# Kernel tuning notes

Measured on AMD Instinct MI355X. Metric: run time of the kernel, lower is better.

## Reference

```python
import jax, jax.numpy as jnp
import numpy as np

B, S, D, H, DH, FF = 2, 2048, 1024, 16, 64, 4096
EPS = 1e-6


def setup_inputs() -> dict:
    key = jax.random.key(0)
    ks = jax.random.split(key, 12)
    s = lambda fan: 1.0 / np.sqrt(fan)
    return {
        "x": jax.random.normal(ks[0], (B, S, D), dtype=jnp.float32),
        "mask": jax.random.randint(ks[1], (B, S), 0, 2).astype(bool),
        "Wq": jax.random.normal(ks[2], (D, H * DH), dtype=jnp.float32) * s(D),
        "Wk": jax.random.normal(ks[3], (D, H * DH), dtype=jnp.float32) * s(D),
        "Wv": jax.random.normal(ks[4], (D, H * DH), dtype=jnp.float32) * s(D),
        "Wo": jax.random.normal(ks[5], (H * DH, D), dtype=jnp.float32) * s(H * DH),
        "bo": jnp.zeros((D,), dtype=jnp.float32),
        "W1": jax.random.normal(ks[6], (D, FF), dtype=jnp.float32) * s(D),
        "b1": jnp.zeros((FF,), dtype=jnp.float32),
        "W2": jax.random.normal(ks[7], (FF, D), dtype=jnp.float32) * s(FF),
        "b2": jnp.zeros((D,), dtype=jnp.float32),
        "g1": jnp.ones((D,), dtype=jnp.float32),   # layer_norm1 target_std
        "m1": jnp.zeros((D,), dtype=jnp.float32),  # layer_norm1 target_mean
        "g2": jnp.ones((D,), dtype=jnp.float32),
        "m2": jnp.zeros((D,), dtype=jnp.float32),
    }


def layer_norm(x, g, m):
    mu = jnp.mean(x, axis=-1, keepdims=True)
    xc = x - mu
    std = jnp.sqrt(jnp.mean(xc * xc, axis=-1, keepdims=True) + EPS)
    return g * xc / std + m


def reference(x, mask, Wq, Wk, Wv, Wo, bo, W1, b1, W2, b2, g1, m1, g2, m2):
    # --- multi-head self-attention (no proj bias) ---
    q = (x @ Wq).reshape(B, S, H, DH)
    k = (x @ Wk).reshape(B, S, H, DH)
    v = (x @ Wv).reshape(B, S, H, DH)
    scores = jnp.einsum("bqhd,bkhd->bhqk", q, k) / np.sqrt(DH)  # [B,H,S,S]
    scores = jnp.where(mask[:, None, None, :], -jnp.inf, scores)
    att = jax.nn.softmax(scores, axis=-1)
    ctx = jnp.einsum("bhqk,bkhd->bqhd", att, v).reshape(B, S, H * DH)
    attn_out = ctx @ Wo + bo
    # --- post-LN residual block (pre_ln=False, dropouts=0 in eval) ---
    x1 = layer_norm(attn_out + x, g1, m1)
    ff = jax.nn.relu(x1 @ W1 + b1) @ W2 + b2
    return layer_norm(ff + x1, g2, m2)
```

## Files before the change

### kernel.cpp

```cpp
#include <hip/hip_runtime.h>
#include <hip/hip_bf16.h>


typedef __bf16 bf16;
typedef __bf16 bf16x8 __attribute__((ext_vector_type(8)));
typedef __bf16 bf16x4 __attribute__((ext_vector_type(4)));
typedef float  f32x4  __attribute__((ext_vector_type(4)));
typedef float  f32x16 __attribute__((ext_vector_type(16)));
typedef unsigned u32x2 __attribute__((ext_vector_type(2)));
typedef unsigned u32x4 __attribute__((ext_vector_type(4)));

#define DEVI __device__ __forceinline__

constexpr int S_LEN  = 2048;
constexpr int NTOK   = 4096;
constexpr int DMODEL = 1024;
constexpr int NFF    = 4096;
constexpr float SCALE2 = 0.125f * 1.44269504088896f;
constexpr float MASKV2 = -30000.0f;

DEVI void gld16(const void* g, void* l) {
  __builtin_amdgcn_global_load_lds((const __attribute__((address_space(1))) void*)g,
                                   (__attribute__((address_space(3))) void*)l, 16, 0, 0);
}

DEVI f32x4 mfma16(bf16x8 a, bf16x8 b, f32x4 c) {
  return __builtin_amdgcn_mfma_f32_16x16x32_bf16(a, b, c, 0, 0, 0);
}
DEVI f32x16 mfma32(bf16x8 a, bf16x8 b, f32x16 c) {
  return __builtin_amdgcn_mfma_f32_32x32x16_bf16(a, b, c, 0, 0, 0);
}
DEVI unsigned cvtpk(float lo, float hi) {
  unsigned d;
  asm("v_cvt_pk_bf16_f32 %0, %1, %2" : "=v"(d) : "v"(lo), "v"(hi));
  return d;
}
DEVI void plswap(unsigned &a, unsigned &b) {
#if __has_builtin(__builtin_amdgcn_permlane32_swap)
  u32x2 r = __builtin_amdgcn_permlane32_swap(a, b, false, false);
  a = r[0]; b = r[1];
#else
  asm volatile("v_permlane32_swap_b32 %0, %1" : "+v"(a), "+v"(b));
#endif
}
DEVI float fexp2(float x) {
#if __has_builtin(__builtin_amdgcn_exp2f)
  return __builtin_amdgcn_exp2f(x);
#else
  return exp2f(x);
#endif
}
#define M3(a, b, c) fmaxf(fmaxf(a, b), c)

template <int MODE>
__global__ __launch_bounds__(512) void gemm8p(
    const bf16* __restrict__ A, const bf16* __restrict__ Bt,
    void* __restrict__ out, const float* __restrict__ bias, int N, int nx)
{
  __shared__ bf16 lds8[65536];
  const int tid = threadIdx.x, lane = tid & 63, w = tid >> 6;
  const int wr = w >> 2, wc = w & 3;
  const int li16 = lane & 15, hi4 = lane >> 4, l7 = lane & 7, b3 = (lane >> 3) & 1;

  const int id = blockIdx.x;
  const int t2 = id >> 3;
  const int bx = t2 % nx;
  const int by = (id & 7) * 2 + t2 / nx;
  const int brow = by * 256, bcol = bx * 256;

  const int srow = tid >> 3;
  const int ssl  = (tid & 7) ^ ((srow ^ (srow >> 3)) & 7);
  const bf16* aG = A  + ((size_t)(brow + srow)) * 1024 + ssl * 8;
  const bf16* bG = Bt + ((size_t)(bcol + srow)) * 1024 + ssl * 8;

  auto STA = [&](int buf, int t, int h) {
    const bf16* g = aG + t * 64 + (size_t)(h * 2) * 65536;
    gld16(g,         lds8 + buf * 32768 + (h * 2) * 4096 + w * 512);
    gld16(g + 65536, lds8 + buf * 32768 + (h * 2 + 1) * 4096 + w * 512);
  };
  auto STB = [&](int buf, int t, int h) {
    const bf16* g = bG + t * 64 + (size_t)(h * 2) * 65536;
    gld16(g,         lds8 + buf * 32768 + 16384 + (h * 2) * 4096 + w * 512);
    gld16(g + 65536, lds8 + buf * 32768 + 16384 + (h * 2 + 1) * 4096 + w * 512);
  };

  const int sa[4] = { l7 ^ ((0 + b3) & 7), l7 ^ ((2 + b3) & 7),
                      l7 ^ ((4 + b3) & 7), l7 ^ ((6 + b3) & 7) };
  const int sb[2] = { l7 ^ ((wc * 4 + 0 + b3) & 7), l7 ^ ((wc * 4 + 2 + b3) & 7) };

  f32x4 acc[2][2][4][2] = {};

#define VM4 asm volatile("s_waitcnt vmcnt(4)" ::: "memory")
#define VM0 asm volatile("s_waitcnt vmcnt(0)" ::: "memory")
#define NOP ((void)0)
#define PH(BUF, MQ, NQ, STG, WAIT) do {                                          \
    bf16x8 af[4][2], bg[2][2];                                                   \
    _Pragma("unroll") for (int m = 0; m < 4; ++m) {                              \
      const bf16* rp = lds8 + (BUF) * 32768 +                                    \
                       ((MQ) * 128 + wr * 64 + m * 16 + li16) * 64;              \
      _Pragma("unroll") for (int ks = 0; ks < 2; ++ks)                           \
        af[m][ks] = *(const bf16x8*)(rp + ((ks * 4 + hi4) ^ sa[m]) * 8);         \
    }                                                                            \
    _Pragma("unroll") for (int n = 0; n < 2; ++n) {                              \
      const bf16* rp = lds8 + (BUF) * 32768 + 16384 +                            \
                       ((NQ) * 128 + wc * 32 + n * 16 + li16) * 64;              \
      _Pragma("unroll") for (int ks = 0; ks < 2; ++ks)                           \
        bg[n][ks] = *(const bf16x8*)(rp + ((ks * 4 + hi4) ^ sb[n]) * 8);         \
    }                                                                            \
    STG;                                                                         \
    asm volatile("s_barrier" ::: "memory");                                      \
    __builtin_amdgcn_s_setprio(1);                                               \
    _Pragma("unroll") for (int m = 0; m < 4; ++m)                                \
      _Pragma("unroll") for (int n = 0; n < 2; ++n)                              \
        _Pragma("unroll") for (int ks = 0; ks < 2; ++ks)                         \
          acc[MQ][NQ][m][n] = mfma16(af[m][ks], bg[n][ks], acc[MQ][NQ][m][n]);   \
    __builtin_amdgcn_s_setprio(0);                                               \
    __builtin_amdgcn_sched_barrier(0);                                           \
    WAIT;                                                                        \
    asm volatile("s_barrier" ::: "memory");                                      \
  } while (0)

  STA(0, 0, 0); STA(0, 0, 1); STB(0, 0, 0); STB(0, 0, 1);
  STA(1, 1, 0); STB(1, 1, 0);
  VM4;
  asm volatile("s_barrier" ::: "memory");

  for (int it = 0; it < 7; ++it) {
    const int t = 2 * it;
    PH(0, 0, 0, STA(1, t + 1, 1), NOP);
    PH(0, 0, 1, STB(1, t + 1, 1), NOP);
    PH(0, 1, 0, STA(0, t + 2, 0), NOP);
    PH(0, 1, 1, STB(0, t + 2, 0), VM4);
    PH(1, 0, 0, STA(0, t + 2, 1), NOP);
    PH(1, 0, 1, STB(0, t + 2, 1), NOP);
    PH(1, 1, 0, STA(1, t + 3, 0), NOP);
    PH(1, 1, 1, STB(1, t + 3, 0), VM4);
  }
  PH(0, 0, 0, STA(1, 15, 1), NOP);
  PH(0, 0, 1, STB(1, 15, 1), NOP);
  PH(0, 1, 0, NOP, NOP);
  PH(0, 1, 1, NOP, VM0);
  PH(1, 0, 0, NOP, NOP);
  PH(1, 0, 1, NOP, NOP);
  PH(1, 1, 0, NOP, NOP);
  PH(1, 1, 1, NOP, NOP);
#undef PH
#undef VM4
#undef VM0
#undef NOP

  const size_t plane = (size_t)NTOK * DMODEL;
#pragma unroll
  for (int mq = 0; mq < 2; ++mq)
#pragma unroll
    for (int nq = 0; nq < 2; ++nq)
#pragma unroll
      for (int m = 0; m < 4; ++m)
#pragma unroll
        for (int n = 0; n < 2; ++n)
#pragma unroll
          for (int j = 0; j < 4; ++j) {
            const int row = brow + mq * 128 + wr * 64 + m * 16 + hi4 * 4 + j;
            const int col = bcol + nq * 128 + wc * 32 + n * 16 + li16;
            const float v = acc[mq][nq][m][n][j];
            if (MODE == 3) {
              const float t = v + bias[col];
              ((bf16*)out)[(size_t)row * N + col] = (bf16)fmaxf(t, 0.0f);
            } else {
              const int b = row >> 11, s = row & 2047;
              const int which = col >> 10, c = col & 1023, h = c >> 6, d = c & 63;
              bf16* qkv = (bf16*)out;
              if (which == 0)
                qkv[(((size_t)(b * 16 + h)) * 2048 + s) * 64 + d] = (bf16)(v * SCALE2);
              else if (which == 1)
                (qkv + plane)[(((size_t)(b * 16 + h)) * 2048 + s) * 64 + d] = (bf16)v;
              else
                (qkv + 2 * plane)[(((size_t)(b * 16 + h)) * 64 + d) * 2048 + s] = (bf16)v;
            }
          }
}

template <int MODE>
__global__ __launch_bounds__(256) void gemm_bt(
    const bf16* __restrict__ A, const bf16* __restrict__ Bt,
    void* __restrict__ out, const float* __restrict__ bias,
    int M, int N, int ld, int Kc, int nx, int ny)
{
  __shared__ bf16 As[128 * 32];
  __shared__ bf16 Bs[128 * 32];
  const int tid  = threadIdx.x;
  const int lane = tid & 63, w = tid >> 6;
  const int wr = w >> 1, wc = w & 1;

  const int id  = blockIdx.x;
  const int xcd = id & 7;
  int t2 = id >> 3;
  const int bx = t2 % nx;  t2 /= nx;
  const int ppx = ny >> 3;
  const int kz = t2 / ppx;
  const int by = xcd * ppx + (t2 % ppx);
  const int brow = by * 128, bcol = bx * 128;

  const bf16* Ag = A  + (size_t)(brow + w * 32 + (lane >> 2)) * ld + kz * Kc + (lane & 3) * 8;
  const bf16* Bg = Bt + (size_t)(bcol + w * 32 + (lane >> 2)) * ld + kz * Kc + (lane & 3) * 8;
  bf16* AsW = As + w * 1024;
  bf16* BsW = Bs + w * 1024;

  f32x4 acc[4][4] = {};

  for (int k0 = 0; k0 < Kc; k0 += 32) {
    gld16(Ag + k0,                    AsW);
    gld16(Ag + k0 + (size_t)16 * ld,  AsW + 512);
    gld16(Bg + k0,                    BsW);
    gld16(Bg + k0 + (size_t)16 * ld,  BsW + 512);
    __syncthreads();

    bf16x8 af[4], bfr[4];
#pragma unroll
    for (int m = 0; m < 4; ++m)
      af[m] = *(const bf16x8*)&As[(wr * 64 + m * 16 + (lane & 15)) * 32 + (lane >> 4) * 8];
#pragma unroll
    for (int n = 0; n < 4; ++n)
      bfr[n] = *(const bf16x8*)&Bs[(wc * 64 + n * 16 + (lane & 15)) * 32 + (lane >> 4) * 8];
    __builtin_amdgcn_s_setprio(1);
#pragma unroll
    for (int m = 0; m < 4; ++m)
#pragma unroll
      for (int n = 0; n < 4; ++n)
        acc[m][n] = mfma16(af[m], bfr[n], acc[m][n]);
    __builtin_amdgcn_s_setprio(0);
    __syncthreads();
  }

#pragma unroll
  for (int m = 0; m < 4; ++m)
#pragma unroll
    for (int n = 0; n < 4; ++n)
#pragma unroll
      for (int r = 0; r < 4; ++r) {
        const int row = brow + wr * 64 + m * 16 + (lane >> 4) * 4 + r;
        const int col = bcol + wc * 64 + n * 16 + (lane & 15);
        ((float*)out)[(size_t)kz * M * N + (size_t)row * N + col] = acc[m][n][r];
      }
}

__global__ __launch_bounds__(512) void attn_k(
    const bf16* __restrict__ q, const bf16* __restrict__ k,
    const bf16* __restrict__ vt, const unsigned* __restrict__ mbits,
    bf16* __restrict__ ctx)
{
  __shared__ __align__(16) char smem[36864];
  bf16* Kl = (bf16*)smem;
  bf16* Vl = (bf16*)(smem + 16384);
  const int tid = threadIdx.x, lane = tid & 63, w = tid >> 6;
  const int hi = lane >> 5, li = lane & 31;
  const int id = blockIdx.x;
  const int j = id >> 3;
  const int bh = (id & 7) * 4 + (j & 3);
  const int b = bh >> 4, h = bh & 15;
  const int qbase = (j >> 2) * 256 + w * 32;

  bf16x8 qf[4];
  {
    const bf16* qp = q + ((size_t)bh * S_LEN + qbase + li) * 64 + hi * 8;
#pragma unroll
    for (int c = 0; c < 4; ++c) qf[c] = *(const bf16x8*)(qp + c * 16);
  }
  const u32x4 onesu = {0x3F803F80u, 0x3F803F80u, 0x3F803F80u, 0x3F803F80u};
  const bf16x8 onesv = __builtin_bit_cast(bf16x8, onesu);

  f32x16 o[2] = {};
  f32x16 acc1 = {};
  float mrun = -3.0e38f;

  const int srow = w * 8 + (lane >> 3);
  const int sslot = (lane & 7) ^ ((srow ^ (srow >> 3)) & 7);
  const bf16* kg = k  + ((size_t)bh * S_LEN + srow) * 64 + sslot * 8;
  const bf16* vg = vt + ((size_t)bh * 64 + srow) * S_LEN + sslot * 8;

  gld16(kg, Kl + w * 512);
  gld16(vg, Vl + w * 512);
  __syncthreads();

  int buf = 0;
  for (int kt = 0; kt < 32; ++kt) {
    const int nb = buf ^ 1;
    if (kt + 1 < 32) {
      gld16(kg + (size_t)(kt + 1) * 4096, Kl + nb * 4096 + w * 512);
      gld16(vg + (kt + 1) * 64,           Vl + nb * 4096 + w * 512);
    }
    const unsigned mw0 = mbits[b * 64 + kt * 2]     >> (hi * 4);
    const unsigned mw1 = mbits[b * 64 + kt * 2 + 1] >> (hi * 4);
    const bf16* Kb = Kl + buf * 4096;
    const bf16* Vb = Vl + buf * 4096;

    float sc[2][16];
#pragma unroll
    for (int kblk = 0; kblk < 2; ++kblk) {
      const int key = kblk * 32 + li;
      const unsigned swb = ((key ^ (key >> 3)) & 7) << 4;
      const char* kr = (const char*)Kb + key * 128;
      f32x16 st = {};
      __builtin_amdgcn_s_setprio(1);
#pragma unroll
      for (int c = 0; c < 4; ++c) {
        const bf16x8 kf = *(const bf16x8*)(kr + ((unsigned)(c * 32 + hi * 16) ^ swb));
        st = mfma32(kf, qf[c], st);
      }
      __builtin_amdgcn_s_setprio(0);
      const unsigned msh = kblk ? mw1 : mw0;
#pragma unroll
      for (int r = 0; r < 16; ++r) {
        const int cb = (r & 3) + 8 * (r >> 2);
        sc[kblk][r] = (msh & (1u << cb)) ? MASKV2 : st[r];
      }
    }

    const float* sf = &sc[0][0];
    float m0[11];
#pragma unroll
    for (int i3 = 0; i3 < 10; ++i3) m0[i3] = M3(sf[i3 * 3], sf[i3 * 3 + 1], sf[i3 * 3 + 2]);
    m0[10] = fmaxf(sf[30], sf[31]);
    float tm = fmaxf(fmaxf(M3(m0[0], m0[1], m0[2]), M3(m0[3], m0[4], m0[5])),
                     fmaxf(M3(m0[6], m0[7], m0[8]), fmaxf(m0[9], m0[10])));
    tm = fmaxf(tm, __shfl_xor(tm, 32, 64));

    if (!__all(tm <= mrun + 11.0f)) {
      const float mnew = fmaxf(mrun, tm);
      const float alpha = fexp2(mrun - mnew);
      mrun = mnew;
      o[0] *= alpha;
      o[1] *= alpha;
      acc1[0] = acc1[0] * alpha;
    }
#pragma unroll
    for (int kblk = 0; kblk < 2; ++kblk)
#pragma unroll
      for (int r = 0; r < 16; ++r)
        sc[kblk][r] = fexp2(sc[kblk][r] - mrun);

    bf16x8 pa[4];
#pragma unroll
    for (int kblk = 0; kblk < 2; ++kblk)
#pragma unroll
      for (int hf = 0; hf < 2; ++hf) {
        unsigned A = cvtpk(sc[kblk][hf * 8 + 0], sc[kblk][hf * 8 + 1]);
        unsigned B = cvtpk(sc[kblk][hf * 8 + 2], sc[kblk][hf * 8 + 3]);
        unsigned C = cvtpk(sc[kblk][hf * 8 + 4], sc[kblk][hf * 8 + 5]);
        unsigned D = cvtpk(sc[kblk][hf * 8 + 6], sc[kblk][hf * 8 + 7]);
        plswap(A, C);
        plswap(B, D);
        const u32x4 t = {A, B, C, D};
        pa[kblk * 2 + hf] = __builtin_bit_cast(bf16x8, t);
      }

#pragma unroll
    for (int dblk = 0; dblk < 2; ++dblk) {
      const int d = dblk * 32 + li;
      const unsigned swb = ((d ^ (d >> 3)) & 7) << 4;
      const char* vr = (const char*)Vb + d * 128;
      __builtin_amdgcn_s_setprio(1);
#pragma unroll
      for (int ch = 0; ch < 4; ++ch) {
        const bf16x8 vf = *(const bf16x8*)(vr + ((unsigned)(ch * 32 + hi * 16) ^ swb));
        o[dblk] = mfma32(vf, pa[ch], o[dblk]);
      }
      __builtin_amdgcn_s_setprio(0);
    }
#pragma unroll
    for (int ch = 0; ch < 4; ++ch) acc1 = mfma32(onesv, pa[ch], acc1);
    __syncthreads();
    buf = nb;
  }

  const float rl = 1.0f / acc1[0];
  char* Ep = smem + w * 4608;
#pragma unroll
  for (int dblk = 0; dblk < 2; ++dblk)
#pragma unroll
    for (int g = 0; g < 4; ++g) {
      const unsigned lo = cvtpk(o[dblk][4 * g + 0] * rl, o[dblk][4 * g + 1] * rl);
      const unsigned hw = cvtpk(o[dblk][4 * g + 2] * rl, o[dblk][4 * g + 3] * rl);
      const int d0 = 8 * g + 4 * hi + 32 * dblk;
      *(unsigned long long*)(Ep + li * 144 + d0 * 2) =
          ((unsigned long long)hw << 32) | (unsigned long long)lo;
    }
#pragma unroll
  for (int i = 0; i < 4; ++i) {
    const int r = (lane >> 3) + 8 * i;
    const bf16x8 vv = *(const bf16x8*)(Ep + r * 144 + (lane & 7) * 16);
    *(bf16x8*)(ctx + ((size_t)b * S_LEN + qbase + r) * DMODEL + h * 64 + (lane & 7) * 8) = vv;
  }
}

template <int NPART, int RB>
__global__ __launch_bounds__(256) void ln_k(
    const float* __restrict__ parts, const float* __restrict__ bias,
    const void* __restrict__ resid, const float* __restrict__ gam,
    const float* __restrict__ bet, float* __restrict__ of, bf16* __restrict__ ob)
{
  const int row = blockIdx.x, t = threadIdx.x;
  float4 v = ((const float4*)(parts + (size_t)row * DMODEL))[t];
#pragma unroll
  for (int p = 1; p < NPART; ++p) {
    const float4 u = ((const float4*)(parts + ((size_t)p * NTOK + row) * DMODEL))[t];
    v.x += u.x; v.y += u.y; v.z += u.z; v.w += u.w;
  }
  {
    const float4 b4 = ((const float4*)bias)[t];
    float4 r4;
    if (RB) {
      const bf16x4 rb = *(const bf16x4*)((const bf16*)resid + (size_t)row * DMODEL + t * 4);
      r4.x = (float)rb[0]; r4.y = (float)rb[1]; r4.z = (float)rb[2]; r4.w = (float)rb[3];
    } else {
      r4 = ((const float4*)((const float*)resid + (size_t)row * DMODEL))[t];
    }
    v.x += b4.x + r4.x; v.y += b4.y + r4.y; v.z += b4.z + r4.z; v.w += b4.w + r4.w;
  }
  float s  = v.x + v.y + v.z + v.w;
  float s2 = v.x * v.x + v.y * v.y + v.z * v.z + v.w * v.w;
#pragma unroll
  for (int off = 1; off < 64; off <<= 1) {
    s  += __shfl_xor(s, off, 64);
    s2 += __shfl_xor(s2, off, 64);
  }
  __shared__ float ps[4], ps2[4];
  if ((t & 63) == 0) { ps[t >> 6] = s; ps2[t >> 6] = s2; }
  __syncthreads();
  s  = ps[0] + ps[1] + ps[2] + ps[3];
  s2 = ps2[0] + ps2[1] + ps2[2] + ps2[3];
  const float mu   = s * (1.f / 1024.f);
  const float var  = fmaxf(s2 * (1.f / 1024.f) - mu * mu, 0.f);
  const float rstd = rsqrtf(var + 1e-6f);
  const float4 g4 = ((const float4*)gam)[t];
  const float4 b4 = ((const float4*)bet)[t];
  float4 ov;
  ov.x = g4.x * (v.x - mu) * rstd + b4.x;
  ov.y = g4.y * (v.y - mu) * rstd + b4.y;
  ov.z = g4.z * (v.z - mu) * rstd + b4.z;
  ov.w = g4.w * (v.w - mu) * rstd + b4.w;
  if (of) ((float4*)(of + (size_t)row * DMODEL))[t] = ov;
  if (ob) {
    const bf16x4 o4 = {(bf16)ov.x, (bf16)ov.y, (bf16)ov.z, (bf16)ov.w};
    *(bf16x4*)(ob + (size_t)row * DMODEL + t * 4) = o4;
  }
}

__global__ __launch_bounds__(256) void prep_k(
    const float* __restrict__ x, const float* __restrict__ Wq,
    const float* __restrict__ Wk, const float* __restrict__ Wv,
    const float* __restrict__ Wo, const float* __restrict__ W1,
    const float* __restrict__ W2, const void* __restrict__ mask,
    bf16* __restrict__ xb, bf16* __restrict__ WqkvT, bf16* __restrict__ WoT,
    bf16* __restrict__ W1T, bf16* __restrict__ W2T, unsigned* __restrict__ mbits)
{
  __shared__ float tile[32][33];
  __shared__ int s_gt1, s_f1;
  const int tid = threadIdx.x;
  const int id = blockIdx.x;

  if (id < 4096) {
    const int i = id * 256 + tid;
    const float4 v = ((const float4*)x)[i];
    const bf16x4 o = {(bf16)v.x, (bf16)v.y, (bf16)v.z, (bf16)v.w};
    *(bf16x4*)(xb + (size_t)i * 4) = o;
    return;
  }
  if (id == 16384) {
    if (tid == 0) { s_gt1 = 0; s_f1 = 0; }
    __syncthreads();
    const unsigned* wds = (const unsigned*)mask;
    int gt1 = 0, f1 = 0;
    for (int i = tid; i < 1024; i += 256) {
      const unsigned xw = wds[i];
      gt1 |= (xw > 1u);
      f1  |= (xw == 0x3F800000u);
    }
    if (gt1) atomicOr(&s_gt1, 1);
    if (f1)  atomicOr(&s_f1, 1);
    __syncthreads();
    const int md = s_f1 ? 2 : (s_gt1 ? 1 : 0);
    if (tid < NTOK / 32) {
      unsigned wd = 0;
      for (int jj = 0; jj < 32; ++jj) {
        const int e = tid * 32 + jj;
        unsigned mv;
        if (md == 1)      mv = (((const unsigned char*)mask)[e] != 0);
        else if (md == 2) mv = (((const float*)mask)[e] != 0.f);
        else              mv = (((const int*)mask)[e] != 0);
        wd |= mv << jj;
      }
      mbits[tid] = wd;
    }
    return;
  }
  const float* src; bf16* dst; int K, N, bx, by;
  if (id < 7168) {
    int s2 = id - 4096; const int wq = s2 >> 10; s2 &= 1023;
    src = wq == 0 ? Wq : (wq == 1 ? Wk : Wv);
    dst = WqkvT + (size_t)wq * DMODEL * DMODEL;
    K = 1024; N = 1024; bx = s2 & 31; by = s2 >> 5;
  } else if (id < 8192) {
    const int s2 = id - 7168;
    src = Wo; dst = WoT; K = 1024; N = 1024; bx = s2 & 31; by = s2 >> 5;
  } else if (id < 12288) {
    const int s2 = id - 8192;
    src = W1; dst = W1T; K = 1024; N = 4096; bx = s2 & 127; by = s2 >> 7;
  } else {
    const int s2 = id - 12288;
    src = W2; dst = W2T; K = 4096; N = 1024; bx = s2 & 31; by = s2 >> 5;
  }
  const int tx = tid & 31, ty = tid >> 5;
  const int r0 = by * 32, c0 = bx * 32;
#pragma unroll
  for (int i = 0; i < 32; i += 8)
    tile[ty + i][tx] = src[(size_t)(r0 + ty + i) * N + c0 + tx];
  __syncthreads();
#pragma unroll
  for (int i = 0; i < 32; i += 8)
    dst[(size_t)(c0 + ty + i) * K + r0 + tx] = (bf16)tile[tx][ty + i];
}

extern "C" void kernel_launch(void* const* d_in, const int* in_sizes, int n_in,
                              void* d_out, int out_size, void* d_ws, size_t ws_size,
                              hipStream_t stream)
{
  const float* x    = (const float*)d_in[0];
  const void*  mask = d_in[1];
  const float* Wq   = (const float*)d_in[2];
  const float* Wk   = (const float*)d_in[3];
  const float* Wv   = (const float*)d_in[4];
  const float* Wo   = (const float*)d_in[5];
  const float* bo   = (const float*)d_in[6];
  const float* W1   = (const float*)d_in[7];
  const float* b1   = (const float*)d_in[8];
  const float* W2   = (const float*)d_in[9];
  const float* b2   = (const float*)d_in[10];
  const float* g1   = (const float*)d_in[11];
  const float* m1   = (const float*)d_in[12];
  const float* g2   = (const float*)d_in[13];
  const float* m2   = (const float*)d_in[14];

  const size_t plane = (size_t)NTOK * DMODEL;

  char* ws = (char*)d_ws;
  size_t off = 0;
  auto alloc = [&](size_t bytes) {
    char* p = ws + off;
    off += (bytes + 255) & ~(size_t)255;
    return p;
  };
  bf16* xb     = (bf16*)alloc(plane * 2);
  bf16* WqkvT  = (bf16*)alloc((size_t)3 * DMODEL * DMODEL * 2);
  bf16* WoT    = (bf16*)alloc((size_t)DMODEL * DMODEL * 2);
  bf16* W1T    = (bf16*)alloc((size_t)NFF * DMODEL * 2);
  bf16* W2T    = (bf16*)alloc((size_t)DMODEL * NFF * 2);
  bf16* qkv    = (bf16*)alloc(4 * plane * 2);
  bf16* qb = qkv, *kb = qkv + plane, *vtb = qkv + 2 * plane, *ctxb = qkv + 3 * plane;
  bf16* hb     = qkv;
  float* parts = (float*)alloc(2 * plane * 4);
  bf16*  x1b   = (bf16*)alloc(plane * 2);
  unsigned* maskbits = (unsigned*)alloc(512);

  prep_k<<<dim3(16385), dim3(256), 0, stream>>>(
      x, Wq, Wk, Wv, Wo, W1, W2, mask, xb, WqkvT, WoT, W1T, W2T, maskbits);

  gemm8p<0><<<dim3(192), dim3(512), 0, stream>>>(xb, WqkvT, qkv, nullptr, 3 * DMODEL, 12);

  attn_k<<<dim3(256), dim3(512), 0, stream>>>(qb, kb, vtb, maskbits, ctxb);

  gemm_bt<4><<<dim3(512), dim3(256), 0, stream>>>(
      ctxb, WoT, parts, nullptr, NTOK, DMODEL, DMODEL, DMODEL / 2, 8, 32);
  ln_k<2, 0><<<dim3(NTOK), dim3(256), 0, stream>>>(parts, bo, x, g1, m1, nullptr, x1b);

  gemm8p<3><<<dim3(256), dim3(512), 0, stream>>>(x1b, W1T, hb, b1, NFF, 16);
  gemm_bt<4><<<dim3(512), dim3(256), 0, stream>>>(
      hb, W2T, parts, nullptr, NTOK, DMODEL, NFF, NFF / 2, 8, 32);
  ln_k<2, 1><<<dim3(NTOK), dim3(256), 0, stream>>>(parts, b2, x1b, g2, m2, (float*)d_out, nullptr);
}
```

Measured before the change: 286.0 us.

## Run FFN down-projection on 8-wave gemm8p with 4-way split-K and merged phases

```diff
diff --git a/kernel.cpp b/kernel.cpp
--- a/kernel.cpp
+++ b/kernel.cpp
@@ -55,7 +55,8 @@
 template <int MODE>
 __global__ __launch_bounds__(512) void gemm8p(
     const bf16* __restrict__ A, const bf16* __restrict__ Bt,
-    void* __restrict__ out, const float* __restrict__ bias, int N, int nx)
+    void* __restrict__ out, const float* __restrict__ bias,
+    int N, int ldA, int ldB, int nx)
 {
   __shared__ bf16 lds8[65536];
   const int tid = threadIdx.x, lane = tid & 63, w = tid >> 6;
@@ -63,25 +64,27 @@
   const int li16 = lane & 15, hi4 = lane >> 4, l7 = lane & 7, b3 = (lane >> 3) & 1;
 
   const int id = blockIdx.x;
-  const int t2 = id >> 3;
-  const int bx = t2 % nx;
-  const int by = (id & 7) * 2 + t2 / nx;
+  const int xcd = id & 7;
+  int t2 = id >> 3;
+  const int bx = t2 % nx;  t2 /= nx;
+  const int kz = t2 >> 1;
+  const int by = xcd * 2 + (t2 & 1);
   const int brow = by * 256, bcol = bx * 256;
 
   const int srow = tid >> 3;
   const int ssl  = (tid & 7) ^ ((srow ^ (srow >> 3)) & 7);
-  const bf16* aG = A  + ((size_t)(brow + srow)) * 1024 + ssl * 8;
-  const bf16* bG = Bt + ((size_t)(bcol + srow)) * 1024 + ssl * 8;
+  const bf16* aG = A  + (size_t)(brow + srow) * ldA + kz * 1024 + ssl * 8;
+  const bf16* bG = Bt + (size_t)(bcol + srow) * ldB + kz * 1024 + ssl * 8;
 
   auto STA = [&](int buf, int t, int h) {
-    const bf16* g = aG + t * 64 + (size_t)(h * 2) * 65536;
-    gld16(g,         lds8 + buf * 32768 + (h * 2) * 4096 + w * 512);
-    gld16(g + 65536, lds8 + buf * 32768 + (h * 2 + 1) * 4096 + w * 512);
+    const bf16* g = aG + t * 64 + (size_t)(h * 128) * ldA;
+    gld16(g,                      lds8 + buf * 32768 + (h * 2) * 4096 + w * 512);
+    gld16(g + (size_t)64 * ldA,   lds8 + buf * 32768 + (h * 2 + 1) * 4096 + w * 512);
   };
   auto STB = [&](int buf, int t, int h) {
-    const bf16* g = bG + t * 64 + (size_t)(h * 2) * 65536;
-    gld16(g,         lds8 + buf * 32768 + 16384 + (h * 2) * 4096 + w * 512);
-    gld16(g + 65536, lds8 + buf * 32768 + 16384 + (h * 2 + 1) * 4096 + w * 512);
+    const bf16* g = bG + t * 64 + (size_t)(h * 128) * ldB;
+    gld16(g,                      lds8 + buf * 32768 + 16384 + (h * 2) * 4096 + w * 512);
+    gld16(g + (size_t)64 * ldB,   lds8 + buf * 32768 + 16384 + (h * 2 + 1) * 4096 + w * 512);
   };
 
   const int sa[4] = { l7 ^ ((0 + b3) & 7), l7 ^ ((2 + b3) & 7),
@@ -89,31 +92,37 @@
   const int sb[2] = { l7 ^ ((wc * 4 + 0 + b3) & 7), l7 ^ ((wc * 4 + 2 + b3) & 7) };
 
   f32x4 acc[2][2][4][2] = {};
+  bf16x8 bg[2][2][2];
 
 #define VM4 asm volatile("s_waitcnt vmcnt(4)" ::: "memory")
 #define VM0 asm volatile("s_waitcnt vmcnt(0)" ::: "memory")
 #define NOP ((void)0)
-#define PH(BUF, MQ, NQ, STG, WAIT) do {                                          \
-    bf16x8 af[4][2], bg[2][2];                                                   \
+#define QPH(BUF, MQ, RDB, STG, WAIT) do {                                        \
+    bf16x8 af[4][2];                                                             \
     _Pragma("unroll") for (int m = 0; m < 4; ++m) {                              \
       const bf16* rp = lds8 + (BUF) * 32768 +                                    \
                        ((MQ) * 128 + wr * 64 + m * 16 + li16) * 64;              \
       _Pragma("unroll") for (int ks = 0; ks < 2; ++ks)                           \
         af[m][ks] = *(const bf16x8*)(rp + ((ks * 4 + hi4) ^ sa[m]) * 8);         \
     }                                                                            \
-    _Pragma("unroll") for (int n = 0; n < 2; ++n) {                              \
-      const bf16* rp = lds8 + (BUF) * 32768 + 16384 +                            \
-                       ((NQ) * 128 + wc * 32 + n * 16 + li16) * 64;              \
-      _Pragma("unroll") for (int ks = 0; ks < 2; ++ks)                           \
-        bg[n][ks] = *(const bf16x8*)(rp + ((ks * 4 + hi4) ^ sb[n]) * 8);         \
+    if (RDB) {                                                                   \
+      _Pragma("unroll") for (int nq = 0; nq < 2; ++nq)                           \
+        _Pragma("unroll") for (int n = 0; n < 2; ++n) {                          \
+          const bf16* rp = lds8 + (BUF) * 32768 + 16384 +                        \
+                           (nq * 128 + wc * 32 + n * 16 + li16) * 64;            \
+          _Pragma("unroll") for (int ks = 0; ks < 2; ++ks)                       \
+            bg[nq][n][ks] = *(const bf16x8*)(rp + ((ks * 4 + hi4) ^ sb[n]) * 8); \
+        }                                                                        \
     }                                                                            \
     STG;                                                                         \
     asm volatile("s_barrier" ::: "memory");                                      \
     __builtin_amdgcn_s_setprio(1);                                               \
-    _Pragma("unroll") for (int m = 0; m < 4; ++m)                                \
-      _Pragma("unroll") for (int n = 0; n < 2; ++n)                              \
-        _Pragma("unroll") for (int ks = 0; ks < 2; ++ks)                         \
-          acc[MQ][NQ][m][n] = mfma16(af[m][ks], bg[n][ks], acc[MQ][NQ][m][n]);   \
+    _Pragma("unroll") for (int nq = 0; nq < 2; ++nq)                             \
+      _Pragma("unroll") for (int m = 0; m < 4; ++m)                              \
+        _Pragma("unroll") for (int n = 0; n < 2; ++n)                            \
+          _Pragma("unroll") for (int ks = 0; ks < 2; ++ks)                       \
+            acc[MQ][nq][m][n] = mfma16(af[m][ks], bg[nq][n][ks],                 \
+                                       acc[MQ][nq][m][n]);                       \
     __builtin_amdgcn_s_setprio(0);                                               \
     __builtin_amdgcn_sched_barrier(0);                                           \
     WAIT;                                                                        \
@@ -127,24 +136,16 @@
 
   for (int it = 0; it < 7; ++it) {
     const int t = 2 * it;
-    PH(0, 0, 0, STA(1, t + 1, 1), NOP);
-    PH(0, 0, 1, STB(1, t + 1, 1), NOP);
-    PH(0, 1, 0, STA(0, t + 2, 0), NOP);
-    PH(0, 1, 1, STB(0, t + 2, 0), VM4);
-    PH(1, 0, 0, STA(0, t + 2, 1), NOP);
-    PH(1, 0, 1, STB(0, t + 2, 1), NOP);
-    PH(1, 1, 0, STA(1, t + 3, 0), NOP);
-    PH(1, 1, 1, STB(1, t + 3, 0), VM4);
-  }
-  PH(0, 0, 0, STA(1, 15, 1), NOP);
-  PH(0, 0, 1, STB(1, 15, 1), NOP);
-  PH(0, 1, 0, NOP, NOP);
-  PH(0, 1, 1, NOP, VM0);
-  PH(1, 0, 0, NOP, NOP);
-  PH(1, 0, 1, NOP, NOP);
-  PH(1, 1, 0, NOP, NOP);
-  PH(1, 1, 1, NOP, NOP);
-#undef PH
+    QPH(0, 0, 1, { STA(1, t + 1, 1); STB(1, t + 1, 1); }, NOP);
+    QPH(0, 1, 0, { STA(0, t + 2, 0); STB(0, t + 2, 0); }, VM4);
+    QPH(1, 0, 1, { STA(0, t + 2, 1); STB(0, t + 2, 1); }, NOP);
+    QPH(1, 1, 0, { STA(1, t + 3, 0); STB(1, t + 3, 0); }, VM4);
+  }
+  QPH(0, 0, 1, { STA(1, 15, 1); STB(1, 15, 1); }, NOP);
+  QPH(0, 1, 0, NOP, VM0);
+  QPH(1, 0, 1, NOP, NOP);
+  QPH(1, 1, 0, NOP, NOP);
+#undef QPH
 #undef VM4
 #undef VM0
 #undef NOP
@@ -166,6 +167,8 @@
             if (MODE == 3) {
               const float t = v + bias[col];
               ((bf16*)out)[(size_t)row * N + col] = (bf16)fmaxf(t, 0.0f);
+            } else if (MODE == 4) {
+              ((float*)out)[(size_t)kz * NTOK * N + (size_t)row * N + col] = v;
             } else {
               const int b = row >> 11, s = row & 2047;
               const int which = col >> 10, c = col & 1023, h = c >> 6, d = c & 63;
@@ -558,14 +561,15 @@
   bf16* qkv    = (bf16*)alloc(4 * plane * 2);
   bf16* qb = qkv, *kb = qkv + plane, *vtb = qkv + 2 * plane, *ctxb = qkv + 3 * plane;
   bf16* hb     = qkv;
-  float* parts = (float*)alloc(2 * plane * 4);
+  float* parts = (float*)alloc(4 * plane * 4);
   bf16*  x1b   = (bf16*)alloc(plane * 2);
   unsigned* maskbits = (unsigned*)alloc(512);
 
   prep_k<<<dim3(16385), dim3(256), 0, stream>>>(
       x, Wq, Wk, Wv, Wo, W1, W2, mask, xb, WqkvT, WoT, W1T, W2T, maskbits);
 
-  gemm8p<0><<<dim3(192), dim3(512), 0, stream>>>(xb, WqkvT, qkv, nullptr, 3 * DMODEL, 12);
+  gemm8p<0><<<dim3(192), dim3(512), 0, stream>>>(
+      xb, WqkvT, qkv, nullptr, 3 * DMODEL, DMODEL, DMODEL, 12);
 
   attn_k<<<dim3(256), dim3(512), 0, stream>>>(qb, kb, vtb, maskbits, ctxb);
 
@@ -573,8 +577,9 @@
       ctxb, WoT, parts, nullptr, NTOK, DMODEL, DMODEL, DMODEL / 2, 8, 32);
   ln_k<2, 0><<<dim3(NTOK), dim3(256), 0, stream>>>(parts, bo, x, g1, m1, nullptr, x1b);
 
-  gemm8p<3><<<dim3(256), dim3(512), 0, stream>>>(x1b, W1T, hb, b1, NFF, 16);
-  gemm_bt<4><<<dim3(512), dim3(256), 0, stream>>>(
-      hb, W2T, parts, nullptr, NTOK, DMODEL, NFF, NFF / 2, 8, 32);
-  ln_k<2, 1><<<dim3(NTOK), dim3(256), 0, stream>>>(parts, b2, x1b, g2, m2, (float*)d_out, nullptr);
-}
+  gemm8p<3><<<dim3(256), dim3(512), 0, stream>>>(
+      x1b, W1T, hb, b1, NFF, DMODEL, DMODEL, 16);
+  gemm8p<4><<<dim3(256), dim3(512), 0, stream>>>(
+      hb, W2T, parts, nullptr, DMODEL, NFF, NFF, 4);
+  ln_k<4, 1><<<dim3(NTOK), dim3(256), 0, stream>>>(parts, b2, x1b, g2, m2, (float*)d_out, nullptr);
+}
```

New measurement: 269.3 us. 5.8% less time.
